# Performance work log

Measured on AMD Instinct MI355X. Metric: run time of the kernel, lower is better.

The kernel has to match this reference:

```python
import math
import jax, jax.numpy as jnp
import numpy as np

BLOCK = 32          # hard-coded in the CUDA kernels
NUM_HEADS = 16
NUM_BLOCKS = 512    # (max_pos//32) * block_per_row = 128 * 4
DIAG_N = 3
FIRST_N = 0


def _mra2_attention(Q, K, V, mask):
    # Q,K,V: (meta_batch, seq, head_dim); mask: (meta_batch, seq) in {0,1}
    mb, seq_len, d = Q.shape
    bs = BLOCK
    nb = seq_len // bs
    scale = 1.0 / math.sqrt(d)
    Q = Q * mask[:, :, None]
    K = K * mask[:, :, None]
    V = V * mask[:, :, None]

    # ---- low resolution block means (mask-weighted), approx_mode='full' keeps V_hat
    tc = mask.reshape(mb, nb, bs).sum(-1)                 # token count per block
    denom = tc[:, :, None] + 1e-6
    Q_hat = Q.reshape(mb, nb, bs, d).sum(2) / denom       # (mb, nb, d)
    K_hat = K.reshape(mb, nb, bs, d).sum(2) / denom
    V_hat = V.reshape(mb, nb, bs, d).sum(2) / denom
    low_logit = jnp.einsum('bid,bjd->bij', Q_hat, K_hat) * scale
    row_max = low_logit.max(-1, keepdims=True)            # before mask subtraction
    low_logit = low_logit - 10000.0 * ((tc[:, None, :] * tc[:, :, None]) < 0.5).astype(Q.dtype)

    # ---- block index selection (torch runs this under no_grad)
    lrn = jax.lax.stop_gradient(low_logit - row_max)
    if DIAG_N > 0:
        off = DIAG_N // 2
        i = jnp.arange(nb)
        band = (jnp.abs(i[:, None] - i[None, :]) <= off).astype(Q.dtype)
        lrn = lrn + band[None] * 5000.0
    if FIRST_N > 0:
        lrn = lrn.at[:, :FIRST_N, :].add(5000.0)
        lrn = lrn.at[:, :, :FIRST_N].add(5000.0)
    top_vals, indices = jax.lax.top_k(lrn.reshape(mb, nb * nb), NUM_BLOCKS)
    threshold = top_vals.min(-1)
    high_mask = (lrn >= threshold[:, None, None]).astype(Q.dtype)  # selected-block mask

    q_blk = indices // nb                                  # (mb, n) query block ids
    k_blk = indices % nb                                   # (mb, n) key block ids
    Qs = jnp.take_along_axis(Q.reshape(mb, nb, bs, d), q_blk[:, :, None, None], axis=1)
    Ks = jnp.take_along_axis(K.reshape(mb, nb, bs, d), k_blk[:, :, None, None], axis=1)
    Vs = jnp.take_along_axis(V.reshape(mb, nb, bs, d), k_blk[:, :, None, None], axis=1)

    # sampled dense-dense: sparse_C[b,n,k,q] (key-in-block, query-in-block layout as in kernel)
    hi_logit = jnp.einsum('bnkd,bnqd->bnkq', Ks, Qs) * scale

    # per query-row max over selected blocks (kernel index_max; constant for grad)
    b_idx = jnp.arange(mb)[:, None]
    blk_max = hi_logit.max(axis=2)                         # (mb, n, bs) max over key axis
    max_blocks = jnp.full((mb, nb, bs), -1e8, Q.dtype).at[b_idx, q_blk].max(blk_max)
    max_blocks = jax.lax.stop_gradient(max_blocks)
    max_vals = max_blocks.reshape(mb, seq_len)
    max_scatter = jnp.take_along_axis(max_blocks, q_blk[:, :, None], axis=1)[:, :, None, :]

    # key-side mask per selected block (sparse_mask_B)
    mask_blk = jnp.take_along_axis(mask.reshape(mb, nb, bs), k_blk[:, :, None], axis=1)
    hi_attn = jnp.exp(hi_logit - max_scatter - 10000.0 * (1.0 - mask_blk[:, :, :, None]))

    # sparse-dense matmul + reduce-sum normalizer, scattered back per query block
    hi_out = jnp.zeros((mb, nb, bs, d), Q.dtype).at[b_idx, q_blk].add(
        jnp.einsum('bnkq,bnkd->bnqd', hi_attn, Vs)).reshape(mb, seq_len, d)
    hi_norm = jnp.zeros((mb, nb, bs), Q.dtype).at[b_idx, q_blk].add(
        hi_attn.sum(axis=2)).reshape(mb, seq_len)

    # ---- low resolution branch, selected blocks suppressed via high_mask
    low_attn = jnp.exp(low_logit - row_max - 10000.0 * high_mask) * tc[:, None, :]
    low_out = jnp.repeat(jnp.einsum('bij,bjd->bid', low_attn, V_hat), bs, axis=1)
    low_norm = jnp.repeat(low_attn.sum(-1), bs, axis=1)

    log_corr = (jnp.repeat(row_max[:, :, 0], bs, axis=1) - max_vals) * mask
    low_corr = jnp.exp(jnp.minimum(log_corr, 0.0))
    hi_corr = jnp.exp(-jnp.maximum(log_corr, 0.0))

    ctx = hi_out * hi_corr[:, :, None] + low_out * low_corr[:, :, None]
    ctx = ctx / (hi_norm * hi_corr + low_norm * low_corr + 1e-6)[:, :, None]
    return ctx * mask[:, :, None]


def _forward(hidden_states, attention_mask, w_q, b_q, w_k, b_k, w_v, b_v):
    b, s, hdim = hidden_states.shape
    h = NUM_HEADS
    dh = hdim // h

    def split_heads(x):
        return x.reshape(b, s, h, dh).transpose(0, 2, 1, 3).reshape(b * h, s, dh)

    q = split_heads(hidden_states @ w_q.T + b_q)
    k = split_heads(hidden_states @ w_k.T + b_k)
    v = split_heads(hidden_states @ w_v.T + b_v)
    # invert extended additive mask (1 + am/10000) and replicate over heads
    # (torch's .repeat(1, h, 1).reshape(b*h, s) stacks h copies of the [b,s] mask)
    mask = jnp.tile(1.0 + attention_mask / 10000.0, (h, 1))
    ctx = _mra2_attention(q, k, v, mask)
    ctx = ctx.reshape(b, h, s, dh).transpose(0, 2, 1, 3).reshape(b, s, hdim)
    return ctx


def setup_inputs() -> dict:
    key = jax.random.key(0)
    ks = jax.random.split(key, 4)
    H = 1024
    return {
        'hidden_states': jax.random.normal(ks[0], (2, 4096, H), jnp.float32),
        'attention_mask': jnp.zeros((2, 4096), jnp.float32),
        'w_q': jax.random.normal(ks[1], (H, H), jnp.float32) * 0.02,
        'b_q': jnp.zeros((H,), jnp.float32),
        'w_k': jax.random.normal(ks[2], (H, H), jnp.float32) * 0.02,
        'b_k': jnp.zeros((H,), jnp.float32),
        'w_v': jax.random.normal(ks[3], (H, H), jnp.float32) * 0.02,
        'b_v': jnp.zeros((H,), jnp.float32),
    }


def reference(hidden_states, attention_mask, w_q, b_q, w_k, b_k, w_v, b_v):
    return _forward(hidden_states, attention_mask, w_q, b_q, w_k, b_k, w_v, b_v)
```

## Files before the change

kernel.cpp:

```cpp
#include <hip/hip_runtime.h>
#include <cstdint>
#include <cstddef>

#define MAXSEL 160
static constexpr int S    = 4096;
static constexpr int H    = 1024;
static constexpr int DH   = 64;
static constexpr int NB   = 128;
static constexpr int MBH  = 32;
static constexpr int M8   = 8192;
static constexpr int N3   = 3072;

typedef _Float16 half8 __attribute__((ext_vector_type(8)));
typedef _Float16 half4v __attribute__((ext_vector_type(4)));
typedef float floatx4 __attribute__((ext_vector_type(4)));

__device__ __forceinline__ void load_lds16(const void* g, void* l) {
  __builtin_amdgcn_global_load_lds((const __attribute__((address_space(1))) unsigned int*)g,
                                   (__attribute__((address_space(3))) unsigned int*)l,
                                   16, 0, 0);
}

__global__ __launch_bounds__(256) void k_prep(const float* __restrict__ hidden,
                                              const float* __restrict__ am,
                                              const float* __restrict__ wq,
                                              const float* __restrict__ wk,
                                              const float* __restrict__ wv,
                                              _Float16* __restrict__ h16,
                                              _Float16* __restrict__ w16,
                                              _Float16* __restrict__ wlo,
                                              _Float16* __restrict__ hb_hi,
                                              _Float16* __restrict__ hb_lo,
                                              float* __restrict__ tcv,
                                              int* __restrict__ selcnt) {
  const int blk_id = blockIdx.x;
  if (blk_id < 256) {
    if (blk_id == 0) {
      for (int i = threadIdx.x; i < MBH * NB; i += 256) selcnt[i] = 0;
    }
    int b2 = blk_id >> 7, blk = blk_id & 127;
    int c = threadIdx.x * 4;
    float4 s0 = make_float4(0.f, 0.f, 0.f, 0.f);
    float4 s1 = make_float4(0.f, 0.f, 0.f, 0.f);
    for (int i = 0; i < 32; i += 4) {
      int pos0 = blk * 32 + i;
      size_t base = ((size_t)b2 * 4096 + pos0) * 1024 + c;
      const float4 x0 = *(const float4*)&hidden[base];
      const float4 x1 = *(const float4*)&hidden[base + 1024];
      const float4 x2 = *(const float4*)&hidden[base + 2048];
      const float4 x3 = *(const float4*)&hidden[base + 3072];
      float a00 = am[pos0],      a01 = am[pos0 + 1],      a02 = am[pos0 + 2],      a03 = am[pos0 + 3];
      float a10 = am[4096+pos0], a11 = am[4096+pos0 + 1], a12 = am[4096+pos0 + 2], a13 = am[4096+pos0 + 3];
      half4v h;
      h[0]=(_Float16)x0.x; h[1]=(_Float16)x0.y; h[2]=(_Float16)x0.z; h[3]=(_Float16)x0.w;
      *(half4v*)&h16[base] = h;
      h[0]=(_Float16)x1.x; h[1]=(_Float16)x1.y; h[2]=(_Float16)x1.z; h[3]=(_Float16)x1.w;
      *(half4v*)&h16[base + 1024] = h;
      h[0]=(_Float16)x2.x; h[1]=(_Float16)x2.y; h[2]=(_Float16)x2.z; h[3]=(_Float16)x2.w;
      *(half4v*)&h16[base + 2048] = h;
      h[0]=(_Float16)x3.x; h[1]=(_Float16)x3.y; h[2]=(_Float16)x3.z; h[3]=(_Float16)x3.w;
      *(half4v*)&h16[base + 3072] = h;
      float m0, m1;
      m0 = 1.f + a00 * 1e-4f; m1 = 1.f + a10 * 1e-4f;
      s0.x += m0*x0.x; s0.y += m0*x0.y; s0.z += m0*x0.z; s0.w += m0*x0.w;
      s1.x += m1*x0.x; s1.y += m1*x0.y; s1.z += m1*x0.z; s1.w += m1*x0.w;
      m0 = 1.f + a01 * 1e-4f; m1 = 1.f + a11 * 1e-4f;
      s0.x += m0*x1.x; s0.y += m0*x1.y; s0.z += m0*x1.z; s0.w += m0*x1.w;
      s1.x += m1*x1.x; s1.y += m1*x1.y; s1.z += m1*x1.z; s1.w += m1*x1.w;
      m0 = 1.f + a02 * 1e-4f; m1 = 1.f + a12 * 1e-4f;
      s0.x += m0*x2.x; s0.y += m0*x2.y; s0.z += m0*x2.z; s0.w += m0*x2.w;
      s1.x += m1*x2.x; s1.y += m1*x2.y; s1.z += m1*x2.z; s1.w += m1*x2.w;
      m0 = 1.f + a03 * 1e-4f; m1 = 1.f + a13 * 1e-4f;
      s0.x += m0*x3.x; s0.y += m0*x3.y; s0.z += m0*x3.z; s0.w += m0*x3.w;
      s1.x += m1*x3.x; s1.y += m1*x3.y; s1.z += m1*x3.z; s1.w += m1*x3.w;
    }
    size_t row0 = (size_t)(b2 * 2 + 0) * 128 + blk;
    size_t row1 = (size_t)(b2 * 2 + 1) * 128 + blk;
    half4v hi, lo;
    hi[0]=(_Float16)s0.x; lo[0]=(_Float16)(s0.x-(float)hi[0]);
    hi[1]=(_Float16)s0.y; lo[1]=(_Float16)(s0.y-(float)hi[1]);
    hi[2]=(_Float16)s0.z; lo[2]=(_Float16)(s0.z-(float)hi[2]);
    hi[3]=(_Float16)s0.w; lo[3]=(_Float16)(s0.w-(float)hi[3]);
    *(half4v*)&hb_hi[row0 * 1024 + c] = hi;
    *(half4v*)&hb_lo[row0 * 1024 + c] = lo;
    hi[0]=(_Float16)s1.x; lo[0]=(_Float16)(s1.x-(float)hi[0]);
    hi[1]=(_Float16)s1.y; lo[1]=(_Float16)(s1.y-(float)hi[1]);
    hi[2]=(_Float16)s1.z; lo[2]=(_Float16)(s1.z-(float)hi[2]);
    hi[3]=(_Float16)s1.w; lo[3]=(_Float16)(s1.w-(float)hi[3]);
    *(half4v*)&hb_hi[row1 * 1024 + c] = hi;
    *(half4v*)&hb_lo[row1 * 1024 + c] = lo;
    if (b2 == 0 && threadIdx.x == 0) {
      float t0 = 0.f, t1 = 0.f;
      for (int i = 0; i < 32; ++i) {
        int pos = blk * 32 + i;
        t0 += 1.f + am[pos] * 1e-4f;
        t1 += 1.f + am[4096 + pos] * 1e-4f;
      }
      tcv[blk] = t0; tcv[128 + blk] = t1;
    }
  } else {
    long j = (long)(blk_id - 256) * 256 + threadIdx.x;
    const long NW4 = (long)H * H / 4;
    int which = (int)(j / NW4);
    long jj = j - (long)which * NW4;
    const float* src = which == 0 ? wq : (which == 1 ? wk : wv);
    float4 x = ((const float4*)src)[jj];
    half4v h;
    h[0] = (_Float16)x.x; h[1] = (_Float16)x.y;
    h[2] = (_Float16)x.z; h[3] = (_Float16)x.w;
    *(half4v*)&w16[j * 4] = h;
    if (which < 2) {
      half4v r;
      r[0] = (_Float16)(x.x - (float)h[0]);
      r[1] = (_Float16)(x.y - (float)h[1]);
      r[2] = (_Float16)(x.z - (float)h[2]);
      r[3] = (_Float16)(x.w - (float)h[3]);
      *(half4v*)&wlo[j * 4] = r;
    }
  }
}

__global__ __launch_bounds__(512, 4) void k_gemm_qkv(const _Float16* __restrict__ A,
                                                     const _Float16* __restrict__ B,
                                                     const float* __restrict__ bq,
                                                     const float* __restrict__ bk,
                                                     const float* __restrict__ bv,
                                                     const float* __restrict__ am,
                                                     _Float16* __restrict__ q16,
                                                     _Float16* __restrict__ k16,
                                                     _Float16* __restrict__ v16) {
  const int id = blockIdx.x;
  const int swz = (id & 7) * 96 + (id >> 3);
  const int by = swz / 12;
  const int bx = swz - by * 12;
  const int tid = threadIdx.x;
  const int lane = tid & 63, wv = tid >> 6;
  const int wm = wv >> 2, wn = wv & 3;
  const int l15 = lane & 15, quad = lane >> 4;

  __shared__ _Float16 As[3][128 * 32];
  __shared__ _Float16 Bs[3][256 * 32];

  floatx4 acc[4][4] = {};

  const _Float16* Ag = A + (size_t)(by * 128) * 1024;
  const _Float16* Bg = B + (size_t)(bx * 256) * 1024;

  const int gr  = lane >> 2;
  const int gcb = ((lane & 3) ^ ((lane >> 3) & 3)) * 8;
  const _Float16* agl  = Ag + (size_t)(wv * 16 + gr) * 1024 + gcb;
  const _Float16* bgl0 = Bg + (size_t)(wv * 32 + gr) * 1024 + gcb;
  const _Float16* bgl1 = Bg + (size_t)(wv * 32 + 16 + gr) * 1024 + gcb;
  const int aw  = (wv * 16) * 32;
  const int bw0 = (wv * 32) * 32;
  const int bw1 = (wv * 32 + 16) * 32;

#define STAGE(TT, BB)                                          \
  {                                                            \
    load_lds16(agl  + (size_t)(TT) * 32, &As[BB][aw]);         \
    load_lds16(bgl0 + (size_t)(TT) * 32, &Bs[BB][bw0]);        \
    load_lds16(bgl1 + (size_t)(TT) * 32, &Bs[BB][bw1]);        \
  }

  STAGE(0, 0)
  STAGE(1, 1)

  const int rc = ((quad ^ ((l15 >> 1) & 3)) << 3);

#pragma unroll
  for (int t = 0; t < 32; ++t) {
    if (t == 31) { asm volatile("s_waitcnt vmcnt(0)" ::: "memory"); }
    else         { asm volatile("s_waitcnt vmcnt(3)" ::: "memory"); }
    __builtin_amdgcn_s_barrier();
    if (t < 30) {
      const int nb = (t + 2) % 3;
      STAGE(t + 2, nb)
    }
    const int bb = t % 3;
    half8 a[4], b[4];
#pragma unroll
    for (int mt = 0; mt < 4; ++mt)
      a[mt] = *(const half8*)&As[bb][(wm * 64 + mt * 16 + l15) * 32 + rc];
#pragma unroll
    for (int nt = 0; nt < 4; ++nt)
      b[nt] = *(const half8*)&Bs[bb][(wn * 64 + nt * 16 + l15) * 32 + rc];
    __builtin_amdgcn_s_setprio(1);
#pragma unroll
    for (int mt = 0; mt < 4; ++mt)
#pragma unroll
      for (int nt = 0; nt < 4; ++nt)
        acc[mt][nt] = __builtin_amdgcn_mfma_f32_16x16x32_f16(a[mt], b[nt], acc[mt][nt], 0, 0, 0);
    __builtin_amdgcn_s_setprio(0);
  }
#undef STAGE

  const int which = bx >> 2;
  const float* bias = which == 0 ? bq : (which == 1 ? bk : bv);
  _Float16* dst = which == 0 ? q16 : (which == 1 ? k16 : v16);
  const int hh = (bx & 3) * 4 + wn;
  const int m2 = hh & 1;
#pragma unroll
  for (int nt = 0; nt < 4; ++nt) {
    const int dd = nt * 16 + l15;
    const float bsv = bias[hh * 64 + dd];
#pragma unroll
    for (int mt = 0; mt < 4; ++mt) {
#pragma unroll
      for (int r = 0; r < 4; ++r) {
        int srow = by * 128 + wm * 64 + mt * 16 + quad * 4 + r;
        int b2 = srow >> 12, s = srow & 4095;
        float mv = 1.f + am[m2 * 4096 + s] * 1e-4f;
        float v = (acc[mt][nt][r] + bsv) * mv;
        int mb = b2 * 16 + hh;
        dst[((size_t)mb * 4096 + s) * 64 + dd] = (_Float16)v;
      }
    }
  }
}

__global__ __launch_bounds__(256) void k_sidev(const _Float16* __restrict__ Ahi,
                                               const _Float16* __restrict__ Alo,
                                               const _Float16* __restrict__ Bhi,
                                               const _Float16* __restrict__ Blo,
                                               float* __restrict__ sideQK,
                                               const _Float16* __restrict__ v16,
                                               const float* __restrict__ tcv,
                                               float* __restrict__ vhat,
                                               _Float16* __restrict__ v16T) {
  __shared__ _Float16 smem[4 * 64 * 64];
  const int tid = threadIdx.x;
  const int lane = tid & 63, wv = tid >> 6;

  if (blockIdx.x >= 512) {
    _Float16* Vs = &smem[wv * 2304];
    int bid = (blockIdx.x - 512) * 4 + wv;
    int mb = bid >> 7, blk = bid & 127;
    const _Float16* src = v16 + ((size_t)mb * 4096 + blk * 32) * 64;
    int r = lane >> 3, c = (lane & 7) * 8;
#pragma unroll
    for (int it = 0; it < 4; ++it)
      *(uint4*)&Vs[(it * 8 + r) * 72 + c] = *(const uint4*)&src[(it * 8 + r) * 64 + c];
    __syncthreads();
    float acc = 0.f;
    half8 col[4];
#pragma unroll
    for (int k = 0; k < 32; ++k) {
      _Float16 x = Vs[k * 72 + lane];
      col[k >> 3][k & 7] = x;
      acc += (float)x;
    }
    vhat[(size_t)bid * 64 + lane] = acc / (tcv[(mb & 1) * 128 + blk] + 1e-6f);
    _Float16* dst = v16T + (size_t)(mb * 64 + lane) * 4096 + blk * 32;
#pragma unroll
    for (int p = 0; p < 4; ++p) *(half8*)&dst[p * 8] = col[p];
    return;
  }

  const int kk = blockIdx.x >> 8;
  const int bb = blockIdx.x & 255;
  const int bx = bb & 31;
  const int by = bb >> 5;
  const int wm = wv >> 1, wn = wv & 1;
  const int l15 = lane & 15, quad = lane >> 4;
  _Float16* sAhi = smem;
  _Float16* sAlo = smem + 4096;
  _Float16* sBhi = smem + 8192;
  _Float16* sBlo = smem + 12288;

  floatx4 acc[2][2] = {};

  const int srow = lane >> 3;
  const int scol = (((lane & 7) ^ (srow & 7)) * 8);
  const int swz  = l15 & 7;
  const _Float16* src;
  _Float16* dst;
  if      (wv == 0) { src = Ahi + (size_t)(by * 64) * 1024; dst = sAhi; }
  else if (wv == 1) { src = Alo + (size_t)(by * 64) * 1024; dst = sAlo; }
  else if (wv == 2) { src = Bhi + (size_t)(bx * 64) * 1024; dst = sBhi; }
  else              { src = Blo + (size_t)(bx * 64) * 1024; dst = sBlo; }

  const int kbeg = kk * 512;
  for (int k0 = kbeg; k0 < kbeg + 512; k0 += 64) {
    __syncthreads();
#pragma unroll
    for (int i = 0; i < 8; ++i)
      load_lds16(src + (size_t)(i * 8 + srow) * 1024 + k0 + scol, dst + i * 512);
    __syncthreads();
#pragma unroll
    for (int ks = 0; ks < 2; ++ks) {
      const int kc = ks * 4;
      half8 ah[2], al[2], bh[2], bl[2];
#pragma unroll
      for (int mt = 0; mt < 2; ++mt) {
        int off = (wm * 32 + mt * 16 + l15) * 64 + (((kc + quad) ^ swz) << 3);
        ah[mt] = *(const half8*)&sAhi[off];
        al[mt] = *(const half8*)&sAlo[off];
      }
#pragma unroll
      for (int nt = 0; nt < 2; ++nt) {
        int off = (wn * 32 + nt * 16 + l15) * 64 + (((kc + quad) ^ swz) << 3);
        bh[nt] = *(const half8*)&sBhi[off];
        bl[nt] = *(const half8*)&sBlo[off];
      }
#pragma unroll
      for (int mt = 0; mt < 2; ++mt)
#pragma unroll
        for (int nt = 0; nt < 2; ++nt) {
          acc[mt][nt] = __builtin_amdgcn_mfma_f32_16x16x32_f16(ah[mt], bh[nt], acc[mt][nt], 0, 0, 0);
          acc[mt][nt] = __builtin_amdgcn_mfma_f32_16x16x32_f16(ah[mt], bl[nt], acc[mt][nt], 0, 0, 0);
          acc[mt][nt] = __builtin_amdgcn_mfma_f32_16x16x32_f16(al[mt], bh[nt], acc[mt][nt], 0, 0, 0);
        }
    }
  }
  float* outp = sideQK + (size_t)kk * (512 * 2048);
#pragma unroll
  for (int mt = 0; mt < 2; ++mt)
#pragma unroll
    for (int nt = 0; nt < 2; ++nt)
#pragma unroll
      for (int rr = 0; rr < 4; ++rr) {
        int row = by * 64 + wm * 32 + mt * 16 + quad * 4 + rr;
        int col = bx * 64 + wn * 32 + nt * 16 + l15;
        outp[(size_t)row * 2048 + col] = acc[mt][nt][rr];
      }
}

__global__ __launch_bounds__(256) void k_lowlogit(const float* __restrict__ sideQK,
                                                  const float* __restrict__ tcv,
                                                  const float* __restrict__ bq,
                                                  const float* __restrict__ bk,
                                                  float* __restrict__ ll,
                                                  float* __restrict__ rmaxout) {
  const int mb = blockIdx.x;
  const int ib = blockIdx.y;
  const int b2 = mb >> 4, m2 = mb & 1, hh = mb & 15;
  const int combo = b2 * 2 + m2;
  const int tid = threadIdx.x;
  __shared__ float Kh[128 * 64];
  __shared__ float Qh[16 * 64];
  __shared__ float tcL[128];

  const float* P1 = sideQK + (size_t)512 * 2048;

  if (tid < 128) tcL[tid] = tcv[m2 * 128 + tid];
  __syncthreads();
#pragma unroll
  for (int i = 0; i < 8; ++i) {
    int ci = tid + i * 256;
    int row = ci >> 4, c4 = (ci & 15) * 4;
    float tck = tcL[row];
    float den = 1.f / (tck + 1e-6f);
    size_t idx = ((size_t)combo * 128 + row) * 2048 + 1024 + hh * 64 + c4;
    float4 x0 = *(const float4*)&sideQK[idx];
    float4 x1 = *(const float4*)&P1[idx];
    float4 bb = *(const float4*)&bk[hh * 64 + c4];
    float4 o;
    o.x = (x0.x + x1.x + bb.x * tck) * den; o.y = (x0.y + x1.y + bb.y * tck) * den;
    o.z = (x0.z + x1.z + bb.z * tck) * den; o.w = (x0.w + x1.w + bb.w * tck) * den;
    *(float4*)&Kh[row * 64 + c4] = o;
  }
  {
    int row = tid >> 4, c4 = (tid & 15) * 4;
    int gi = ib * 16 + row;
    float tcq = tcL[gi];
    float den = 1.f / (tcq + 1e-6f);
    size_t idx = ((size_t)combo * 128 + gi) * 2048 + hh * 64 + c4;
    float4 x0 = *(const float4*)&sideQK[idx];
    float4 x1 = *(const float4*)&P1[idx];
    float4 bb = *(const float4*)&bq[hh * 64 + c4];
    float4 o;
    o.x = (x0.x + x1.x + bb.x * tcq) * den; o.y = (x0.y + x1.y + bb.y * tcq) * den;
    o.z = (x0.z + x1.z + bb.z * tcq) * den; o.w = (x0.w + x1.w + bb.w * tcq) * den;
    *(float4*)&Qh[row * 64 + c4] = o;
  }
  __syncthreads();

  const int il = tid >> 4, jg = tid & 15;
  const int i = ib * 16 + il;
  float tcq = tcL[i];
  float dots[8] = {};
#pragma unroll
  for (int dd = 0; dd < 16; ++dd) {
    int d4 = ((dd + tid) & 15) * 4;
    float4 qv = *(const float4*)&Qh[il * 64 + d4];
#pragma unroll
    for (int jj = 0; jj < 8; ++jj) {
      float4 kv = *(const float4*)&Kh[(jg * 8 + jj) * 64 + d4];
      dots[jj] += qv.x * kv.x + qv.y * kv.y + qv.z * kv.z + qv.w * kv.w;
    }
  }
  float tmax = -1e30f;
#pragma unroll
  for (int jj = 0; jj < 8; ++jj) {
    int j = jg * 8 + jj;
    float raw = dots[jj] * 0.125f;
    tmax = fmaxf(tmax, raw);
    float pen = (tcq * tcL[j] < 0.5f) ? 10000.f : 0.f;
    ll[(size_t)mb * 16384 + (size_t)i * 128 + j] = raw - pen;
  }
#pragma unroll
  for (int mk = 1; mk < 16; mk <<= 1) tmax = fmaxf(tmax, __shfl_xor(tmax, mk));
  if (jg == 0) rmaxout[mb * 128 + i] = tmax;
}

__global__ __launch_bounds__(256) void k_topk(const float* __restrict__ ll,
                                              const float* __restrict__ rmax,
                                              float* __restrict__ thr,
                                              int* __restrict__ selcnt,
                                              int* __restrict__ selkb) {
  const int mb = blockIdx.x;
  const int t = threadIdx.x;
  const int wid = t >> 6;
  __shared__ int red2[2][4];

  unsigned code[64];
#pragma unroll
  for (int j = 0; j < 64; ++j) {
    int e = j * 256 + t;
    int i = e >> 7, jj = e & 127;
    float lrn = ll[(size_t)mb * 16384 + e] - rmax[mb * 128 + i];
    int di = i - jj;
    if (di <= 1 && di >= -1) lrn += 5000.f;
    unsigned b = __float_as_uint(lrn);
    code[j] = (b & 0x80000000u) ? ~b : (b | 0x80000000u);
  }

  unsigned lo = 0u, hi = 0xFFFFFFFFu;
  for (int it = 0; it < 32; ++it) {
    unsigned mid = lo + ((hi - lo) >> 1);
    int c = 0;
#pragma unroll
    for (int j = 0; j < 64; ++j) c += (code[j] >= mid) ? 1 : 0;
#pragma unroll
    for (int mk = 1; mk < 64; mk <<= 1) c += __shfl_xor(c, mk);
    if ((t & 63) == 0) red2[it & 1][wid] = c;
    __syncthreads();
    int total = red2[it & 1][0] + red2[it & 1][1] + red2[it & 1][2] + red2[it & 1][3];
    if (total >= 512) lo = mid; else hi = mid;
  }
  if (t == 0) {
    unsigned bits = (lo & 0x80000000u) ? (lo & 0x7FFFFFFFu) : ~lo;
    thr[mb] = __uint_as_float(bits);
  }
#pragma unroll
  for (int j = 0; j < 64; ++j) {
    if (code[j] >= lo) {
      int e = j * 256 + t;
      int i = e >> 7, jj = e & 127;
      int slot = atomicAdd(&selcnt[mb * 128 + i], 1);
      if (slot < MAXSEL) selkb[(size_t)(mb * 128 + i) * MAXSEL + slot] = jj;
    }
  }
}

__global__ __launch_bounds__(64) void k_hi(const _Float16* __restrict__ q16,
                                           const _Float16* __restrict__ k16,
                                           const _Float16* __restrict__ v16T,
                                           const int* __restrict__ selcnt,
                                           const int* __restrict__ selkb,
                                           const float* __restrict__ rmax,
                                           const float* __restrict__ thr,
                                           const float* __restrict__ tcv,
                                           const float* __restrict__ vhat,
                                           const float* __restrict__ ll,
                                           const float* __restrict__ am,
                                           float* __restrict__ out) {
  const int mb = blockIdx.x & 31, qb = blockIdx.x >> 5;
  const int sid = mb * 128 + qb;
  const int lane = threadIdx.x;
  const int l15 = lane & 15, quad = lane >> 4;
  const int m2 = mb & 1, b2 = mb >> 4, hh = mb & 15;

  __shared__ _Float16 Ps[32 * 40];

  const _Float16* qbase = q16 + ((size_t)mb * 4096 + qb * 32) * 64;
  half8 aq[2][2];
#pragma unroll
  for (int mt = 0; mt < 2; ++mt)
#pragma unroll
    for (int ks = 0; ks < 2; ++ks)
      aq[mt][ks] = *(const half8*)&qbase[(mt * 16 + l15) * 64 + ks * 32 + quad * 8];

  const float rmaxb = rmax[sid];
  const float th = thr[mb];
  float accL = 0.f, nrmL = 0.f;
#pragma unroll 4
  for (int j = 0; j < 128; ++j) {
    float llv = ll[(size_t)mb * 16384 + (size_t)qb * 128 + j];
    float lrn = llv - rmaxb;
    int di = qb - j;
    if (di <= 1 && di >= -1) lrn += 5000.f;
    float w = (lrn >= th) ? 0.f : __expf(llv - rmaxb) * tcv[m2 * 128 + j];
    accL += w * vhat[((size_t)(mb * 128 + j)) * 64 + lane];
    nrmL += w;
  }

  int nk = selcnt[sid];
  if (nk > MAXSEL) nk = MAXSEL;
  const int* list = selkb + (size_t)sid * MAXSEL;

  const _Float16* kbase  = k16  + (size_t)mb * 4096 * 64;
  const _Float16* vtbase = v16T + (size_t)mb * 64 * 4096;

  float rm[2][4];
  floatx4 o[2][4] = {};
  floatx4 onrm[2] = {};
#pragma unroll
  for (int mt = 0; mt < 2; ++mt)
#pragma unroll
    for (int r = 0; r < 4; ++r) rm[mt][r] = -1e8f;

  half8 ones;
#pragma unroll
  for (int j = 0; j < 8; ++j) ones[j] = (_Float16)1.f;

  for (int t = 0; t < nk; ++t) {
    const int kb = list[t];
    const _Float16* kp = kbase + (size_t)kb * 32 * 64;
    half8 b0[2], b1[2];
#pragma unroll
    for (int ks = 0; ks < 2; ++ks) {
      b0[ks] = *(const half8*)&kp[(l15) * 64 + ks * 32 + quad * 8];
      b1[ks] = *(const half8*)&kp[(16 + l15) * 64 + ks * 32 + quad * 8];
    }
    const _Float16* vp = vtbase + kb * 32 + quad * 8;
    half8 vb0 = *(const half8*)&vp[(size_t)(l15) * 4096];
    half8 vb1 = *(const half8*)&vp[(size_t)(16 + l15) * 4096];
    half8 vb2 = *(const half8*)&vp[(size_t)(32 + l15) * 4096];
    half8 vb3 = *(const half8*)&vp[(size_t)(48 + l15) * 4096];

    floatx4 sf[2][2] = {};
    sf[0][0] = __builtin_amdgcn_mfma_f32_16x16x32_f16(aq[0][0], b0[0], sf[0][0], 0, 0, 0);
    sf[0][0] = __builtin_amdgcn_mfma_f32_16x16x32_f16(aq[0][1], b0[1], sf[0][0], 0, 0, 0);
    sf[0][1] = __builtin_amdgcn_mfma_f32_16x16x32_f16(aq[0][0], b1[0], sf[0][1], 0, 0, 0);
    sf[0][1] = __builtin_amdgcn_mfma_f32_16x16x32_f16(aq[0][1], b1[1], sf[0][1], 0, 0, 0);
    sf[1][0] = __builtin_amdgcn_mfma_f32_16x16x32_f16(aq[1][0], b0[0], sf[1][0], 0, 0, 0);
    sf[1][0] = __builtin_amdgcn_mfma_f32_16x16x32_f16(aq[1][1], b0[1], sf[1][0], 0, 0, 0);
    sf[1][1] = __builtin_amdgcn_mfma_f32_16x16x32_f16(aq[1][0], b1[0], sf[1][1], 0, 0, 0);
    sf[1][1] = __builtin_amdgcn_mfma_f32_16x16x32_f16(aq[1][1], b1[1], sf[1][1], 0, 0, 0);

    float pen0, pen1;
    {
      float mk0 = 1.f + am[m2 * 4096 + kb * 32 + l15] * 1e-4f;
      float mk1 = 1.f + am[m2 * 4096 + kb * 32 + 16 + l15] * 1e-4f;
      pen0 = 10000.f * (1.f - mk0);
      pen1 = 10000.f * (1.f - mk1);
    }
#pragma unroll
    for (int mt = 0; mt < 2; ++mt)
#pragma unroll
      for (int r = 0; r < 4; ++r) {
        float s0 = sf[mt][0][r] * 0.125f;
        float s1 = sf[mt][1][r] * 0.125f;
        float v = fmaxf(s0, s1);
#pragma unroll
        for (int mk = 1; mk < 16; mk <<= 1) v = fmaxf(v, __shfl_xor(v, mk));
        float mnew  = fmaxf(rm[mt][r], v);
        float alpha = __expf(rm[mt][r] - mnew);
        rm[mt][r] = mnew;
        float p0 = __expf(s0 - mnew - pen0);
        float p1 = __expf(s1 - mnew - pen1);
        o[mt][0][r] *= alpha; o[mt][1][r] *= alpha;
        o[mt][2][r] *= alpha; o[mt][3][r] *= alpha;
        onrm[mt][r] *= alpha;
        int row = mt * 16 + quad * 4 + r;
        Ps[row * 40 + l15] = (_Float16)p0;
        Ps[row * 40 + 16 + l15] = (_Float16)p1;
      }
    __syncthreads();
    half8 pa0 = *(const half8*)&Ps[(l15) * 40 + quad * 8];
    half8 pa1 = *(const half8*)&Ps[(16 + l15) * 40 + quad * 8];
    o[0][0] = __builtin_amdgcn_mfma_f32_16x16x32_f16(pa0, vb0, o[0][0], 0, 0, 0);
    o[0][1] = __builtin_amdgcn_mfma_f32_16x16x32_f16(pa0, vb1, o[0][1], 0, 0, 0);
    o[0][2] = __builtin_amdgcn_mfma_f32_16x16x32_f16(pa0, vb2, o[0][2], 0, 0, 0);
    o[0][3] = __builtin_amdgcn_mfma_f32_16x16x32_f16(pa0, vb3, o[0][3], 0, 0, 0);
    o[1][0] = __builtin_amdgcn_mfma_f32_16x16x32_f16(pa1, vb0, o[1][0], 0, 0, 0);
    o[1][1] = __builtin_amdgcn_mfma_f32_16x16x32_f16(pa1, vb1, o[1][1], 0, 0, 0);
    o[1][2] = __builtin_amdgcn_mfma_f32_16x16x32_f16(pa1, vb2, o[1][2], 0, 0, 0);
    o[1][3] = __builtin_amdgcn_mfma_f32_16x16x32_f16(pa1, vb3, o[1][3], 0, 0, 0);
    onrm[0] = __builtin_amdgcn_mfma_f32_16x16x32_f16(pa0, ones, onrm[0], 0, 0, 0);
    onrm[1] = __builtin_amdgcn_mfma_f32_16x16x32_f16(pa1, ones, onrm[1], 0, 0, 0);
    __syncthreads();
  }

  float lo_d[4];
#pragma unroll
  for (int ntd = 0; ntd < 4; ++ntd) lo_d[ntd] = __shfl(accL, ntd * 16 + l15);
#pragma unroll
  for (int mt = 0; mt < 2; ++mt) {
#pragma unroll
    for (int r = 0; r < 4; ++r) {
      int q = mt * 16 + quad * 4 + r;
      int qpos = qb * 32 + q;
      float mq = 1.f + am[m2 * 4096 + qpos] * 1e-4f;
      float logc = (rmaxb - rm[mt][r]) * mq;
      float lc = __expf(fminf(logc, 0.f));
      float hc = __expf(-fmaxf(logc, 0.f));
      float den = onrm[mt][r] * hc + nrmL * lc + 1e-6f;
      float sc = mq / den;
#pragma unroll
      for (int ntd = 0; ntd < 4; ++ntd) {
        float val = (o[mt][ntd][r] * hc + lo_d[ntd] * lc) * sc;
        out[((size_t)b2 * 4096 + qpos) * 1024 + hh * 64 + ntd * 16 + l15] = val;
      }
    }
  }
}

extern "C" void kernel_launch(void* const* d_in, const int* in_sizes, int n_in,
                              void* d_out, int out_size, void* d_ws, size_t ws_size,
                              hipStream_t stream) {
  const float* hidden = (const float*)d_in[0];
  const float* am     = (const float*)d_in[1];
  const float* wq     = (const float*)d_in[2];
  const float* bq     = (const float*)d_in[3];
  const float* wk     = (const float*)d_in[4];
  const float* bk     = (const float*)d_in[5];
  const float* wv     = (const float*)d_in[6];
  const float* bv     = (const float*)d_in[7];
  float* out = (float*)d_out;

  char* ws = (char*)d_ws;
  size_t off = 0;
  auto alloc = [&](size_t bytes) -> char* {
    char* p = ws + off;
    off += (bytes + 255) & ~(size_t)255;
    return p;
  };
  _Float16* h16    = (_Float16*)alloc((size_t)M8 * H * 2);
  _Float16* w16    = (_Float16*)alloc((size_t)N3 * H * 2);
  _Float16* wlo    = (_Float16*)alloc((size_t)2 * H * H * 2);
  _Float16* q16    = (_Float16*)alloc((size_t)MBH * S * DH * 2);
  _Float16* k16    = (_Float16*)alloc((size_t)MBH * S * DH * 2);
  _Float16* v16    = (_Float16*)alloc((size_t)MBH * S * DH * 2);
  _Float16* hb_hi  = (_Float16*)alloc((size_t)4 * NB * H * 2);
  _Float16* hb_lo  = (_Float16*)alloc((size_t)4 * NB * H * 2);
  float* tcv       = (float*)alloc((size_t)2 * NB * 4);
  float* sideQK    = (float*)alloc((size_t)2 * 512 * 2048 * 4);
  float* ll        = (float*)alloc((size_t)MBH * NB * NB * 4);
  float* rmax      = (float*)alloc((size_t)MBH * NB * 4);
  float* thr       = (float*)alloc((size_t)MBH * 4);
  int*   selcnt    = (int*)alloc((size_t)MBH * NB * 4);
  int*   selkb     = (int*)alloc((size_t)MBH * NB * MAXSEL * 4);
  float* vhat      = (float*)alloc((size_t)MBH * NB * DH * 4);
  _Float16* v16T   = h16;

  k_prep<<<dim3(3328), dim3(256), 0, stream>>>(hidden, am, wq, wk, wv,
                                               h16, w16, wlo, hb_hi, hb_lo, tcv, selcnt);
  k_gemm_qkv<<<dim3(768), dim3(512), 0, stream>>>(h16, w16, bq, bk, bv, am,
                                                  q16, k16, v16);
  k_sidev<<<dim3(512 + 1024), dim3(256), 0, stream>>>(hb_hi, hb_lo, w16, wlo, sideQK,
                                                      v16, tcv, vhat, v16T);
  k_lowlogit<<<dim3(32, 8), dim3(256), 0, stream>>>(sideQK, tcv, bq, bk, ll, rmax);
  k_topk<<<dim3(32), dim3(256), 0, stream>>>(ll, rmax, thr, selcnt, selkb);
  k_hi<<<dim3(4096), dim3(64), 0, stream>>>(q16, k16, v16T, selcnt, selkb, rmax, thr,
                                            tcv, vhat, ll, am, out);
}
```

Before: 307.9 us.

## Restructure QKV GEMM to 256-thread blocks with 256x128 tiles and split MFMA phases

The QKV projection GEMM drops from 8 to 4 waves per workgroup, and the tile shape changes from 128x256 to 256x128. Each wave now owns a 128x64 output slice with 32 accumulators. The inner loop is split into two halves with extra barriers and lgkmcnt waits, so LDS reads are interleaved with MFMA bursts in a ping-pong style. The LDS swizzle pattern is also changed. The intent is more register-level reuse of the B fragments per wave, at the cost of higher register pressure, more barriers and lower occupancy.

```diff
diff --git a/kernel.cpp b/kernel.cpp
--- a/kernel.cpp
+++ b/kernel.cpp
@@ -120,7 +120,7 @@
   }
 }
 
-__global__ __launch_bounds__(512, 4) void k_gemm_qkv(const _Float16* __restrict__ A,
+__global__ __launch_bounds__(256, 2) void k_gemm_qkv(const _Float16* __restrict__ A,
                                                      const _Float16* __restrict__ B,
                                                      const float* __restrict__ bq,
                                                      const float* __restrict__ bk,
@@ -131,46 +131,47 @@
                                                      _Float16* __restrict__ v16) {
   const int id = blockIdx.x;
   const int swz = (id & 7) * 96 + (id >> 3);
-  const int by = swz / 12;
-  const int bx = swz - by * 12;
+  const int by = swz / 24;
+  const int bx = swz - by * 24;
   const int tid = threadIdx.x;
   const int lane = tid & 63, wv = tid >> 6;
-  const int wm = wv >> 2, wn = wv & 3;
+  const int wm = wv >> 1, wn = wv & 1;
   const int l15 = lane & 15, quad = lane >> 4;
 
-  __shared__ _Float16 As[3][128 * 32];
-  __shared__ _Float16 Bs[3][256 * 32];
-
-  floatx4 acc[4][4] = {};
-
-  const _Float16* Ag = A + (size_t)(by * 128) * 1024;
-  const _Float16* Bg = B + (size_t)(bx * 256) * 1024;
+  __shared__ _Float16 As[3][256 * 32];
+  __shared__ _Float16 Bs[3][128 * 32];
+
+  floatx4 acc[8][4] = {};
+
+  const _Float16* Ag = A + (size_t)(by * 256) * 1024;
+  const _Float16* Bg = B + (size_t)(bx * 128) * 1024;
 
   const int gr  = lane >> 2;
-  const int gcb = ((lane & 3) ^ ((lane >> 3) & 3)) * 8;
-  const _Float16* agl  = Ag + (size_t)(wv * 16 + gr) * 1024 + gcb;
-  const _Float16* bgl0 = Bg + (size_t)(wv * 32 + gr) * 1024 + gcb;
-  const _Float16* bgl1 = Bg + (size_t)(wv * 32 + 16 + gr) * 1024 + gcb;
-  const int aw  = (wv * 16) * 32;
-  const int bw0 = (wv * 32) * 32;
-  const int bw1 = (wv * 32 + 16) * 32;
-
-#define STAGE(TT, BB)                                          \
-  {                                                            \
-    load_lds16(agl  + (size_t)(TT) * 32, &As[BB][aw]);         \
-    load_lds16(bgl0 + (size_t)(TT) * 32, &Bs[BB][bw0]);        \
-    load_lds16(bgl1 + (size_t)(TT) * 32, &Bs[BB][bw1]);        \
+  const int gcb = ((lane & 3) ^ (gr & 3)) * 8;
+  const _Float16* agl = Ag + (size_t)(wv * 64 + gr) * 1024 + gcb;
+  const _Float16* bgl = Bg + (size_t)(wv * 32 + gr) * 1024 + gcb;
+  const int aw = (wv * 64) * 32;
+  const int bw = (wv * 32) * 32;
+
+#define STAGE(TT, BB)                                                        \
+  {                                                                          \
+    load_lds16(agl + (size_t)(TT) * 32,               &As[BB][aw]);          \
+    load_lds16(agl + (size_t)(TT) * 32 + 16 * 1024,   &As[BB][aw + 512]);    \
+    load_lds16(agl + (size_t)(TT) * 32 + 32 * 1024,   &As[BB][aw + 1024]);   \
+    load_lds16(agl + (size_t)(TT) * 32 + 48 * 1024,   &As[BB][aw + 1536]);   \
+    load_lds16(bgl + (size_t)(TT) * 32,               &Bs[BB][bw]);          \
+    load_lds16(bgl + (size_t)(TT) * 32 + 16 * 1024,   &Bs[BB][bw + 512]);    \
   }
 
   STAGE(0, 0)
   STAGE(1, 1)
 
-  const int rc = ((quad ^ ((l15 >> 1) & 3)) << 3);
+  const int rg = ((quad ^ (l15 & 3)) << 3);
 
 #pragma unroll
   for (int t = 0; t < 32; ++t) {
     if (t == 31) { asm volatile("s_waitcnt vmcnt(0)" ::: "memory"); }
-    else         { asm volatile("s_waitcnt vmcnt(3)" ::: "memory"); }
+    else         { asm volatile("s_waitcnt vmcnt(6)" ::: "memory"); }
     __builtin_amdgcn_s_barrier();
     if (t < 30) {
       const int nb = (t + 2) % 3;
@@ -180,10 +181,12 @@
     half8 a[4], b[4];
 #pragma unroll
     for (int mt = 0; mt < 4; ++mt)
-      a[mt] = *(const half8*)&As[bb][(wm * 64 + mt * 16 + l15) * 32 + rc];
+      a[mt] = *(const half8*)&As[bb][(wm * 128 + mt * 16 + l15) * 32 + rg];
 #pragma unroll
     for (int nt = 0; nt < 4; ++nt)
-      b[nt] = *(const half8*)&Bs[bb][(wn * 64 + nt * 16 + l15) * 32 + rc];
+      b[nt] = *(const half8*)&Bs[bb][(wn * 64 + nt * 16 + l15) * 32 + rg];
+    __builtin_amdgcn_s_barrier();
+    asm volatile("s_waitcnt lgkmcnt(0)" ::: "memory");
     __builtin_amdgcn_s_setprio(1);
 #pragma unroll
     for (int mt = 0; mt < 4; ++mt)
@@ -191,23 +194,36 @@
       for (int nt = 0; nt < 4; ++nt)
         acc[mt][nt] = __builtin_amdgcn_mfma_f32_16x16x32_f16(a[mt], b[nt], acc[mt][nt], 0, 0, 0);
     __builtin_amdgcn_s_setprio(0);
+    __builtin_amdgcn_s_barrier();
+#pragma unroll
+    for (int mt = 0; mt < 4; ++mt)
+      a[mt] = *(const half8*)&As[bb][(wm * 128 + (mt + 4) * 16 + l15) * 32 + rg];
+    __builtin_amdgcn_s_barrier();
+    asm volatile("s_waitcnt lgkmcnt(0)" ::: "memory");
+    __builtin_amdgcn_s_setprio(1);
+#pragma unroll
+    for (int mt = 0; mt < 4; ++mt)
+#pragma unroll
+      for (int nt = 0; nt < 4; ++nt)
+        acc[mt + 4][nt] = __builtin_amdgcn_mfma_f32_16x16x32_f16(a[mt], b[nt], acc[mt + 4][nt], 0, 0, 0);
+    __builtin_amdgcn_s_setprio(0);
   }
 #undef STAGE
 
-  const int which = bx >> 2;
+  const int which = bx >> 3;
   const float* bias = which == 0 ? bq : (which == 1 ? bk : bv);
   _Float16* dst = which == 0 ? q16 : (which == 1 ? k16 : v16);
-  const int hh = (bx & 3) * 4 + wn;
+  const int hh = (bx & 7) * 2 + wn;
   const int m2 = hh & 1;
 #pragma unroll
   for (int nt = 0; nt < 4; ++nt) {
     const int dd = nt * 16 + l15;
     const float bsv = bias[hh * 64 + dd];
 #pragma unroll
-    for (int mt = 0; mt < 4; ++mt) {
+    for (int mt = 0; mt < 8; ++mt) {
 #pragma unroll
       for (int r = 0; r < 4; ++r) {
-        int srow = by * 128 + wm * 64 + mt * 16 + quad * 4 + r;
+        int srow = by * 256 + wm * 128 + mt * 16 + quad * 4 + r;
         int b2 = srow >> 12, s = srow & 4095;
         float mv = 1.f + am[m2 * 4096 + s] * 1e-4f;
         float v = (acc[mt][nt][r] + bsv) * mv;
@@ -647,7 +663,7 @@
 
   k_prep<<<dim3(3328), dim3(256), 0, stream>>>(hidden, am, wq, wk, wv,
                                                h16, w16, wlo, hb_hi, hb_lo, tcv, selcnt);
-  k_gemm_qkv<<<dim3(768), dim3(512), 0, stream>>>(h16, w16, bq, bk, bv, am,
+  k_gemm_qkv<<<dim3(768), dim3(256), 0, stream>>>(h16, w16, bq, bk, bv, am,
                                                   q16, k16, v16);
   k_sidev<<<dim3(512 + 1024), dim3(256), 0, stream>>>(hb_hi, hb_lo, w16, wlo, sideQK,
                                                       v16, tcv, vhat, v16T);
```

Result: slower. 322.6 us (+4.8%).

## Merge side GEMM into QKV GEMM launch and V transpose into low-logit kernel

Applied to the files above, without the earlier changes.

Moves the split-precision side GEMM (block sums against weights) into extra blocks of the QKV GEMM launch, with two 256-thread sub-tiles per 512-thread block, so it runs concurrently with the main GEMM instead of in a separate launch. The V block-mean and transpose work moves into k_lowlogit as extra blocks, which removes one kernel launch and lets independent work overlap. The cost is a shared LDS array sized for the larger GEMM, which may limit occupancy, and heterogeneous blocks within one launch.

```diff
diff --git a/kernel.cpp b/kernel.cpp
--- a/kernel.cpp
+++ b/kernel.cpp
@@ -128,112 +128,194 @@
                                                      const float* __restrict__ am,
                                                      _Float16* __restrict__ q16,
                                                      _Float16* __restrict__ k16,
-                                                     _Float16* __restrict__ v16) {
-  const int id = blockIdx.x;
-  const int swz = (id & 7) * 96 + (id >> 3);
-  const int by = swz / 12;
-  const int bx = swz - by * 12;
+                                                     _Float16* __restrict__ v16,
+                                                     const _Float16* __restrict__ Ahi,
+                                                     const _Float16* __restrict__ Alo,
+                                                     const _Float16* __restrict__ Blo,
+                                                     float* __restrict__ sideQK) {
+  __shared__ _Float16 sh[36864];
+
+  if (blockIdx.x < 768) {
+    const int id = blockIdx.x;
+    const int swz = (id & 7) * 96 + (id >> 3);
+    const int by = swz / 12;
+    const int bx = swz - by * 12;
+    const int tid = threadIdx.x;
+    const int lane = tid & 63, wv = tid >> 6;
+    const int wm = wv >> 2, wn = wv & 3;
+    const int l15 = lane & 15, quad = lane >> 4;
+
+    _Float16* As = sh;
+    _Float16* Bs = sh + 12288;
+
+    floatx4 acc[4][4] = {};
+
+    const _Float16* Ag = A + (size_t)(by * 128) * 1024;
+    const _Float16* Bg = B + (size_t)(bx * 256) * 1024;
+
+    const int gr  = lane >> 2;
+    const int gcb = ((lane & 3) ^ ((lane >> 3) & 3)) * 8;
+    const _Float16* agl  = Ag + (size_t)(wv * 16 + gr) * 1024 + gcb;
+    const _Float16* bgl0 = Bg + (size_t)(wv * 32 + gr) * 1024 + gcb;
+    const _Float16* bgl1 = Bg + (size_t)(wv * 32 + 16 + gr) * 1024 + gcb;
+    const int aw  = (wv * 16) * 32;
+    const int bw0 = (wv * 32) * 32;
+    const int bw1 = (wv * 32 + 16) * 32;
+
+#define STAGE(TT, BB)                                                   \
+    {                                                                   \
+      load_lds16(agl  + (size_t)(TT) * 32, &As[(BB) * 4096 + aw]);      \
+      load_lds16(bgl0 + (size_t)(TT) * 32, &Bs[(BB) * 8192 + bw0]);     \
+      load_lds16(bgl1 + (size_t)(TT) * 32, &Bs[(BB) * 8192 + bw1]);     \
+    }
+
+    STAGE(0, 0)
+    STAGE(1, 1)
+
+    const int rc = ((quad ^ ((l15 >> 1) & 3)) << 3);
+
+#pragma unroll
+    for (int t = 0; t < 32; ++t) {
+      if (t == 31) { asm volatile("s_waitcnt vmcnt(0)" ::: "memory"); }
+      else         { asm volatile("s_waitcnt vmcnt(3)" ::: "memory"); }
+      __builtin_amdgcn_s_barrier();
+      if (t < 30) {
+        const int nb = (t + 2) % 3;
+        STAGE(t + 2, nb)
+      }
+      const int bb = t % 3;
+      half8 a[4], b[4];
+#pragma unroll
+      for (int mt = 0; mt < 4; ++mt)
+        a[mt] = *(const half8*)&As[bb * 4096 + (wm * 64 + mt * 16 + l15) * 32 + rc];
+#pragma unroll
+      for (int nt = 0; nt < 4; ++nt)
+        b[nt] = *(const half8*)&Bs[bb * 8192 + (wn * 64 + nt * 16 + l15) * 32 + rc];
+      __builtin_amdgcn_s_setprio(1);
+#pragma unroll
+      for (int mt = 0; mt < 4; ++mt)
+#pragma unroll
+        for (int nt = 0; nt < 4; ++nt)
+          acc[mt][nt] = __builtin_amdgcn_mfma_f32_16x16x32_f16(a[mt], b[nt], acc[mt][nt], 0, 0, 0);
+      __builtin_amdgcn_s_setprio(0);
+    }
+#undef STAGE
+
+    const int which = bx >> 2;
+    const float* bias = which == 0 ? bq : (which == 1 ? bk : bv);
+    _Float16* dst = which == 0 ? q16 : (which == 1 ? k16 : v16);
+    const int hh = (bx & 3) * 4 + wn;
+    const int m2 = hh & 1;
+#pragma unroll
+    for (int nt = 0; nt < 4; ++nt) {
+      const int dd = nt * 16 + l15;
+      const float bsv = bias[hh * 64 + dd];
+#pragma unroll
+      for (int mt = 0; mt < 4; ++mt) {
+#pragma unroll
+        for (int r = 0; r < 4; ++r) {
+          int srow = by * 128 + wm * 64 + mt * 16 + quad * 4 + r;
+          int b2 = srow >> 12, s = srow & 4095;
+          float mv = 1.f + am[m2 * 4096 + s] * 1e-4f;
+          float v = (acc[mt][nt][r] + bsv) * mv;
+          int mb = b2 * 16 + hh;
+          dst[((size_t)mb * 4096 + s) * 64 + dd] = (_Float16)v;
+        }
+      }
+    }
+    return;
+  }
+
+  const int half = threadIdx.x >> 8;
+  const int stid = threadIdx.x & 255;
+  const int sb   = (blockIdx.x - 768) * 2 + half;
+  const int slane = stid & 63, swv = stid >> 6;
+  const int kk  = sb >> 8;
+  const int sbb = sb & 255;
+  const int sbx = sbb & 31;
+  const int sby = sbb >> 5;
+  const int swm = swv >> 1, swn = swv & 1;
+  const int sl15 = slane & 15, squad = slane >> 4;
+  _Float16* base = sh + half * 16384;
+  _Float16* sAhi = base;
+  _Float16* sAlo = base + 4096;
+  _Float16* sBhi = base + 8192;
+  _Float16* sBlo = base + 12288;
+
+  floatx4 acc[2][2] = {};
+
+  const int srow = slane >> 3;
+  const int scol = (((slane & 7) ^ (srow & 7)) * 8);
+  const int sswz = sl15 & 7;
+  const _Float16* src;
+  _Float16* dst;
+  if      (swv == 0) { src = Ahi + (size_t)(sby * 64) * 1024; dst = sAhi; }
+  else if (swv == 1) { src = Alo + (size_t)(sby * 64) * 1024; dst = sAlo; }
+  else if (swv == 2) { src = B   + (size_t)(sbx * 64) * 1024; dst = sBhi; }
+  else               { src = Blo + (size_t)(sbx * 64) * 1024; dst = sBlo; }
+
+  const int kbeg = kk * 512;
+  for (int k0 = kbeg; k0 < kbeg + 512; k0 += 64) {
+    __syncthreads();
+#pragma unroll
+    for (int i = 0; i < 8; ++i)
+      load_lds16(src + (size_t)(i * 8 + srow) * 1024 + k0 + scol, dst + i * 512);
+    __syncthreads();
+#pragma unroll
+    for (int ks = 0; ks < 2; ++ks) {
+      const int kc = ks * 4;
+      half8 ah[2], al[2], bh[2], bl[2];
+#pragma unroll
+      for (int mt = 0; mt < 2; ++mt) {
+        int off = (swm * 32 + mt * 16 + sl15) * 64 + (((kc + squad) ^ sswz) << 3);
+        ah[mt] = *(const half8*)&sAhi[off];
+        al[mt] = *(const half8*)&sAlo[off];
+      }
+#pragma unroll
+      for (int nt = 0; nt < 2; ++nt) {
+        int off = (swn * 32 + nt * 16 + sl15) * 64 + (((kc + squad) ^ sswz) << 3);
+        bh[nt] = *(const half8*)&sBhi[off];
+        bl[nt] = *(const half8*)&sBlo[off];
+      }
+#pragma unroll
+      for (int mt = 0; mt < 2; ++mt)
+#pragma unroll
+        for (int nt = 0; nt < 2; ++nt) {
+          acc[mt][nt] = __builtin_amdgcn_mfma_f32_16x16x32_f16(ah[mt], bh[nt], acc[mt][nt], 0, 0, 0);
+          acc[mt][nt] = __builtin_amdgcn_mfma_f32_16x16x32_f16(ah[mt], bl[nt], acc[mt][nt], 0, 0, 0);
+          acc[mt][nt] = __builtin_amdgcn_mfma_f32_16x16x32_f16(al[mt], bh[nt], acc[mt][nt], 0, 0, 0);
+        }
+    }
+  }
+  float* outp = sideQK + (size_t)kk * (512 * 2048);
+#pragma unroll
+  for (int mt = 0; mt < 2; ++mt)
+#pragma unroll
+    for (int nt = 0; nt < 2; ++nt)
+#pragma unroll
+      for (int rr = 0; rr < 4; ++rr) {
+        int row = sby * 64 + swm * 32 + mt * 16 + squad * 4 + rr;
+        int col = sbx * 64 + swn * 32 + nt * 16 + sl15;
+        outp[(size_t)row * 2048 + col] = acc[mt][nt][rr];
+      }
+}
+
+__global__ __launch_bounds__(256) void k_lowlogit(const float* __restrict__ sideQK,
+                                                  const float* __restrict__ tcv,
+                                                  const float* __restrict__ bq,
+                                                  const float* __restrict__ bk,
+                                                  float* __restrict__ ll,
+                                                  float* __restrict__ rmaxout,
+                                                  const _Float16* __restrict__ v16,
+                                                  float* __restrict__ vhat,
+                                                  _Float16* __restrict__ v16T) {
+  __shared__ __attribute__((aligned(16))) char shraw[37376];
   const int tid = threadIdx.x;
-  const int lane = tid & 63, wv = tid >> 6;
-  const int wm = wv >> 2, wn = wv & 3;
-  const int l15 = lane & 15, quad = lane >> 4;
-
-  __shared__ _Float16 As[3][128 * 32];
-  __shared__ _Float16 Bs[3][256 * 32];
-
-  floatx4 acc[4][4] = {};
-
-  const _Float16* Ag = A + (size_t)(by * 128) * 1024;
-  const _Float16* Bg = B + (size_t)(bx * 256) * 1024;
-
-  const int gr  = lane >> 2;
-  const int gcb = ((lane & 3) ^ ((lane >> 3) & 3)) * 8;
-  const _Float16* agl  = Ag + (size_t)(wv * 16 + gr) * 1024 + gcb;
-  const _Float16* bgl0 = Bg + (size_t)(wv * 32 + gr) * 1024 + gcb;
-  const _Float16* bgl1 = Bg + (size_t)(wv * 32 + 16 + gr) * 1024 + gcb;
-  const int aw  = (wv * 16) * 32;
-  const int bw0 = (wv * 32) * 32;
-  const int bw1 = (wv * 32 + 16) * 32;
-
-#define STAGE(TT, BB)                                          \
-  {                                                            \
-    load_lds16(agl  + (size_t)(TT) * 32, &As[BB][aw]);         \
-    load_lds16(bgl0 + (size_t)(TT) * 32, &Bs[BB][bw0]);        \
-    load_lds16(bgl1 + (size_t)(TT) * 32, &Bs[BB][bw1]);        \
-  }
-
-  STAGE(0, 0)
-  STAGE(1, 1)
-
-  const int rc = ((quad ^ ((l15 >> 1) & 3)) << 3);
-
-#pragma unroll
-  for (int t = 0; t < 32; ++t) {
-    if (t == 31) { asm volatile("s_waitcnt vmcnt(0)" ::: "memory"); }
-    else         { asm volatile("s_waitcnt vmcnt(3)" ::: "memory"); }
-    __builtin_amdgcn_s_barrier();
-    if (t < 30) {
-      const int nb = (t + 2) % 3;
-      STAGE(t + 2, nb)
-    }
-    const int bb = t % 3;
-    half8 a[4], b[4];
-#pragma unroll
-    for (int mt = 0; mt < 4; ++mt)
-      a[mt] = *(const half8*)&As[bb][(wm * 64 + mt * 16 + l15) * 32 + rc];
-#pragma unroll
-    for (int nt = 0; nt < 4; ++nt)
-      b[nt] = *(const half8*)&Bs[bb][(wn * 64 + nt * 16 + l15) * 32 + rc];
-    __builtin_amdgcn_s_setprio(1);
-#pragma unroll
-    for (int mt = 0; mt < 4; ++mt)
-#pragma unroll
-      for (int nt = 0; nt < 4; ++nt)
-        acc[mt][nt] = __builtin_amdgcn_mfma_f32_16x16x32_f16(a[mt], b[nt], acc[mt][nt], 0, 0, 0);
-    __builtin_amdgcn_s_setprio(0);
-  }
-#undef STAGE
-
-  const int which = bx >> 2;
-  const float* bias = which == 0 ? bq : (which == 1 ? bk : bv);
-  _Float16* dst = which == 0 ? q16 : (which == 1 ? k16 : v16);
-  const int hh = (bx & 3) * 4 + wn;
-  const int m2 = hh & 1;
-#pragma unroll
-  for (int nt = 0; nt < 4; ++nt) {
-    const int dd = nt * 16 + l15;
-    const float bsv = bias[hh * 64 + dd];
-#pragma unroll
-    for (int mt = 0; mt < 4; ++mt) {
-#pragma unroll
-      for (int r = 0; r < 4; ++r) {
-        int srow = by * 128 + wm * 64 + mt * 16 + quad * 4 + r;
-        int b2 = srow >> 12, s = srow & 4095;
-        float mv = 1.f + am[m2 * 4096 + s] * 1e-4f;
-        float v = (acc[mt][nt][r] + bsv) * mv;
-        int mb = b2 * 16 + hh;
-        dst[((size_t)mb * 4096 + s) * 64 + dd] = (_Float16)v;
-      }
-    }
-  }
-}
-
-__global__ __launch_bounds__(256) void k_sidev(const _Float16* __restrict__ Ahi,
-                                               const _Float16* __restrict__ Alo,
-                                               const _Float16* __restrict__ Bhi,
-                                               const _Float16* __restrict__ Blo,
-                                               float* __restrict__ sideQK,
-                                               const _Float16* __restrict__ v16,
-                                               const float* __restrict__ tcv,
-                                               float* __restrict__ vhat,
-                                               _Float16* __restrict__ v16T) {
-  __shared__ _Float16 smem[4 * 64 * 64];
-  const int tid = threadIdx.x;
-  const int lane = tid & 63, wv = tid >> 6;
-
-  if (blockIdx.x >= 512) {
-    _Float16* Vs = &smem[wv * 2304];
-    int bid = (blockIdx.x - 512) * 4 + wv;
+
+  if (blockIdx.x >= 256) {
+    const int lane = tid & 63, wv = tid >> 6;
+    _Float16* Vs = (_Float16*)shraw + wv * 2304;
+    int bid = (blockIdx.x - 256) * 4 + wv;
     int mb = bid >> 7, blk = bid & 127;
     const _Float16* src = v16 + ((size_t)mb * 4096 + blk * 32) * 64;
     int r = lane >> 3, c = (lane & 7) * 8;
@@ -256,89 +338,13 @@
     return;
   }
 
-  const int kk = blockIdx.x >> 8;
-  const int bb = blockIdx.x & 255;
-  const int bx = bb & 31;
-  const int by = bb >> 5;
-  const int wm = wv >> 1, wn = wv & 1;
-  const int l15 = lane & 15, quad = lane >> 4;
-  _Float16* sAhi = smem;
-  _Float16* sAlo = smem + 4096;
-  _Float16* sBhi = smem + 8192;
-  _Float16* sBlo = smem + 12288;
-
-  floatx4 acc[2][2] = {};
-
-  const int srow = lane >> 3;
-  const int scol = (((lane & 7) ^ (srow & 7)) * 8);
-  const int swz  = l15 & 7;
-  const _Float16* src;
-  _Float16* dst;
-  if      (wv == 0) { src = Ahi + (size_t)(by * 64) * 1024; dst = sAhi; }
-  else if (wv == 1) { src = Alo + (size_t)(by * 64) * 1024; dst = sAlo; }
-  else if (wv == 2) { src = Bhi + (size_t)(bx * 64) * 1024; dst = sBhi; }
-  else              { src = Blo + (size_t)(bx * 64) * 1024; dst = sBlo; }
-
-  const int kbeg = kk * 512;
-  for (int k0 = kbeg; k0 < kbeg + 512; k0 += 64) {
-    __syncthreads();
-#pragma unroll
-    for (int i = 0; i < 8; ++i)
-      load_lds16(src + (size_t)(i * 8 + srow) * 1024 + k0 + scol, dst + i * 512);
-    __syncthreads();
-#pragma unroll
-    for (int ks = 0; ks < 2; ++ks) {
-      const int kc = ks * 4;
-      half8 ah[2], al[2], bh[2], bl[2];
-#pragma unroll
-      for (int mt = 0; mt < 2; ++mt) {
-        int off = (wm * 32 + mt * 16 + l15) * 64 + (((kc + quad) ^ swz) << 3);
-        ah[mt] = *(const half8*)&sAhi[off];
-        al[mt] = *(const half8*)&sAlo[off];
-      }
-#pragma unroll
-      for (int nt = 0; nt < 2; ++nt) {
-        int off = (wn * 32 + nt * 16 + l15) * 64 + (((kc + quad) ^ swz) << 3);
-        bh[nt] = *(const half8*)&sBhi[off];
-        bl[nt] = *(const half8*)&sBlo[off];
-      }
-#pragma unroll
-      for (int mt = 0; mt < 2; ++mt)
-#pragma unroll
-        for (int nt = 0; nt < 2; ++nt) {
-          acc[mt][nt] = __builtin_amdgcn_mfma_f32_16x16x32_f16(ah[mt], bh[nt], acc[mt][nt], 0, 0, 0);
-          acc[mt][nt] = __builtin_amdgcn_mfma_f32_16x16x32_f16(ah[mt], bl[nt], acc[mt][nt], 0, 0, 0);
-          acc[mt][nt] = __builtin_amdgcn_mfma_f32_16x16x32_f16(al[mt], bh[nt], acc[mt][nt], 0, 0, 0);
-        }
-    }
-  }
-  float* outp = sideQK + (size_t)kk * (512 * 2048);
-#pragma unroll
-  for (int mt = 0; mt < 2; ++mt)
-#pragma unroll
-    for (int nt = 0; nt < 2; ++nt)
-#pragma unroll
-      for (int rr = 0; rr < 4; ++rr) {
-        int row = by * 64 + wm * 32 + mt * 16 + quad * 4 + rr;
-        int col = bx * 64 + wn * 32 + nt * 16 + l15;
-        outp[(size_t)row * 2048 + col] = acc[mt][nt][rr];
-      }
-}
-
-__global__ __launch_bounds__(256) void k_lowlogit(const float* __restrict__ sideQK,
-                                                  const float* __restrict__ tcv,
-                                                  const float* __restrict__ bq,
-                                                  const float* __restrict__ bk,
-                                                  float* __restrict__ ll,
-                                                  float* __restrict__ rmaxout) {
-  const int mb = blockIdx.x;
-  const int ib = blockIdx.y;
+  const int mb = blockIdx.x >> 3;
+  const int ib = blockIdx.x & 7;
   const int b2 = mb >> 4, m2 = mb & 1, hh = mb & 15;
   const int combo = b2 * 2 + m2;
-  const int tid = threadIdx.x;
-  __shared__ float Kh[128 * 64];
-  __shared__ float Qh[16 * 64];
-  __shared__ float tcL[128];
+  float* Kh  = (float*)shraw;
+  float* Qh  = (float*)(shraw + 32768);
+  float* tcL = (float*)(shraw + 32768 + 4096);
 
   const float* P1 = sideQK + (size_t)512 * 2048;
 
@@ -647,11 +653,11 @@
 
   k_prep<<<dim3(3328), dim3(256), 0, stream>>>(hidden, am, wq, wk, wv,
                                                h16, w16, wlo, hb_hi, hb_lo, tcv, selcnt);
-  k_gemm_qkv<<<dim3(768), dim3(512), 0, stream>>>(h16, w16, bq, bk, bv, am,
-                                                  q16, k16, v16);
-  k_sidev<<<dim3(512 + 1024), dim3(256), 0, stream>>>(hb_hi, hb_lo, w16, wlo, sideQK,
-                                                      v16, tcv, vhat, v16T);
-  k_lowlogit<<<dim3(32, 8), dim3(256), 0, stream>>>(sideQK, tcv, bq, bk, ll, rmax);
+  k_gemm_qkv<<<dim3(1024), dim3(512), 0, stream>>>(h16, w16, bq, bk, bv, am,
+                                                   q16, k16, v16,
+                                                   hb_hi, hb_lo, wlo, sideQK);
+  k_lowlogit<<<dim3(1280), dim3(256), 0, stream>>>(sideQK, tcv, bq, bk, ll, rmax,
+                                                   v16, vhat, v16T);
   k_topk<<<dim3(32), dim3(256), 0, stream>>>(ll, rmax, thr, selcnt, selkb);
   k_hi<<<dim3(4096), dim3(64), 0, stream>>>(q16, k16, v16T, selcnt, selkb, rmax, thr,
                                             tcv, vhat, ll, am, out);
```

After: 295.2 us. 1.04x faster.
